# Performance work log

Measured on AMD Instinct MI355X. Metric: run time of the kernel, lower is better.

## Reference

```python
import jax, jax.numpy as jnp
import numpy as np
from jax import lax

W = 65536  # wavelength batch
L = 64     # number of stacked layers
N_IN = 1.0
N_OUT = 1.45
PURITY = 0.87
CD_SCALE = 32980.0  # mdeg conversion, as in source
LN10 = 2.302585092994046


def setup_inputs() -> dict:
    key = jax.random.key(0)
    ks = jax.random.split(key, 9)
    wl = jnp.linspace(0.4, 0.8, W, dtype=jnp.float32)  # microns, matches wl_range*1e-6 usage
    thickP = jax.random.normal(ks[0], (L,), jnp.float32) * 2.0

    def u(k, lo, hi):
        return lo + (hi - lo) * jax.random.uniform(k, (W, L), jnp.float32)

    return {
        "wl": wl,
        "thickP": thickP,
        "mind": jnp.float32(20.0),   # nm
        "maxd": jnp.float32(300.0),  # nm
        "eps_c_re": u(ks[1], 1.8, 4.5),
        "eps_c_im": u(ks[2], 0.0, 0.08),
        "kappa_c_re": u(ks[3], -5e-3, 5e-3),
        "kappa_c_im": u(ks[4], -5e-3, 5e-3),
        "eps_a_re": u(ks[5], 1.8, 4.5),
        "eps_a_im": u(ks[6], 0.0, 0.08),
        "kappa_a_re": u(ks[7], -5e-3, 5e-3),
        "kappa_a_im": u(ks[8], -5e-3, 5e-3),
    }


def _chain(Ms):
    # Ms: [L, W, 2, 2] complex; sequential layer chain-multiply (TMM recursion)
    eye = jnp.broadcast_to(jnp.eye(2, dtype=Ms.dtype), (Ms.shape[1], 2, 2))

    def step(carry, Ml):
        return jnp.einsum('wij,wjk->wik', carry, Ml), None

    Mt, _ = lax.scan(step, eye, Ms)
    return Mt  # [W, 2, 2]


def _absorbance(eps, kappa, sigma, k0, d):
    # Circular eigenmode TMM for Pasteur (isotropic chiral) layers at normal incidence.
    # eps, kappa: [W, L] complex relative quantities; k0: [W]; d: [L] meters.
    n0 = jnp.sqrt(eps)                       # background index, also wave admittance
    n_sig = n0 + sigma * kappa               # circular eigenmode index n +/- kappa
    delta = k0[:, None] * n_sig * d[None, :]  # [W, L] phase thickness
    c = jnp.cos(delta)
    s = jnp.sin(delta)
    Y = n0
    # characteristic matrix per layer: [[cos d, i sin d / Y], [i Y sin d, cos d]]
    M = jnp.stack([jnp.stack([c, 1j * s / Y], axis=-1),
                   jnp.stack([1j * Y * s, c], axis=-1)], axis=-2)  # [W, L, 2, 2]
    Mt = _chain(jnp.transpose(M, (1, 0, 2, 3)))
    m00, m01 = Mt[:, 0, 0], Mt[:, 0, 1]
    m10, m11 = Mt[:, 1, 0], Mt[:, 1, 1]
    denom = N_IN * (m00 + m01 * N_OUT) + (m10 + m11 * N_OUT)
    t = 2.0 * N_IN / denom
    T = (N_OUT / N_IN) * (jnp.abs(t) ** 2)
    return -jnp.log(T + 1e-12) / LN10  # absorbance per handedness


def _stack_cd_abs(eps_re, eps_im, kap_re, kap_im, k0, d):
    eps = (eps_re + 1j * eps_im).astype(jnp.complex64)
    kap = (kap_re + 1j * kap_im).astype(jnp.complex64)
    A_r = _absorbance(eps, kap, +1.0, k0, d)  # RCP
    A_l = _absorbance(eps, kap, -1.0, k0, d)  # LCP
    return A_l - A_r, 0.5 * (A_l + A_r)


def reference(wl, thickP, mind, maxd, eps_c_re, eps_c_im, kappa_c_re, kappa_c_im,
              eps_a_re, eps_a_im, kappa_a_re, kappa_a_im):
    d = (jax.nn.sigmoid(thickP) * (maxd - mind) + mind) * 1e-9  # [L] meters
    k0 = (2.0 * np.float32(3.1415926)) / (wl * 1e-6)             # [W]
    cd_c, abs_c = _stack_cd_abs(eps_c_re, eps_c_im, kappa_c_re, kappa_c_im, k0, d)
    cd_a, abs_a = _stack_cd_abs(eps_a_re, eps_a_im, kappa_a_re, kappa_a_im, k0, d)
    scale = (2.0 * PURITY - 1.0) * CD_SCALE
    return (cd_c * scale, cd_a * scale, abs_c, abs_a)
```

## Files before the change

### kernel.cpp

```cpp
#include <hip/hip_runtime.h>
#include <math.h>

#define LTOT 64
#define GL   8
#define LPL  (LTOT / GL)

#define INV2PI  0.15915494309189535f
#define LOG2E   1.4426950408889634f
#define LOG10_2 0.30102999566398120f

struct cpx { float r, i; };
struct Mat { cpx e00, e01, e10, e11; };

__device__ __forceinline__ cpx cmul(cpx a, cpx b) {
    return { fmaf(a.r, b.r, -a.i * b.i), fmaf(a.r, b.i, a.i * b.r) };
}
__device__ __forceinline__ cpx cmadd(cpx a, cpx b, cpx c) {
    return { fmaf(a.r, b.r, fmaf(-a.i, b.i, c.r)),
             fmaf(a.r, b.i, fmaf( a.i, b.r, c.i)) };
}
__device__ __forceinline__ Mat mmul(const Mat& A, const Mat& B) {
    Mat C;
    C.e00 = cmadd(A.e01, B.e10, cmul(A.e00, B.e00));
    C.e01 = cmadd(A.e01, B.e11, cmul(A.e00, B.e01));
    C.e10 = cmadd(A.e11, B.e10, cmul(A.e10, B.e00));
    C.e11 = cmadd(A.e11, B.e11, cmul(A.e10, B.e01));
    return C;
}
__device__ __forceinline__ void csqrt_inv(cpx z, cpx& n0, float& inv) {
    float m = __builtin_amdgcn_sqrtf(fmaf(z.r, z.r, z.i * z.i));
    float x = 0.5f * (m + z.r);
    float t = __builtin_amdgcn_rsqf(x);
    n0.r = x * t;
    n0.i = 0.5f * z.i * t;
    inv  = __builtin_amdgcn_rcpf(m);
}

__device__ __forceinline__ void accum(Mat& P, bool first, float xrev, float y,
                                      cpx n0, float inv_n0sq) {
    float rf = __builtin_amdgcn_fractf(xrev);
    float s_ = __builtin_amdgcn_sinf(rf);
    float c_ = __builtin_amdgcn_cosf(rf);
    float y2 = y * y;
    float chv = fmaf(y2, fmaf(y2, 0.0416666667f, 0.5f), 1.0f);
    float shv = y * fmaf(y2, fmaf(y2, 0.0083333333f, 0.1666666667f), 1.0f);
    cpx cc = { c_ * chv, -s_ * shv };
    cpx ss = { s_ * chv,  c_ * shv };
    cpx qq = { (ss.r * n0.r + ss.i * n0.i) * inv_n0sq,
               (ss.i * n0.r - ss.r * n0.i) * inv_n0sq };
    cpx m01 = { -qq.i, qq.r };
    cpx p   = cmul(n0, ss);
    cpx m10 = { -p.i, p.r };
    if (first) {
        P.e00 = cc; P.e01 = m01; P.e10 = m10; P.e11 = cc;
    } else {
        Mat C;
        C.e00 = cmadd(P.e01, m10, cmul(P.e00, cc));
        C.e01 = cmadd(P.e01, cc,  cmul(P.e00, m01));
        C.e10 = cmadd(P.e11, m10, cmul(P.e10, cc));
        C.e11 = cmadd(P.e11, cc,  cmul(P.e10, m01));
        P = C;
    }
}

__device__ __forceinline__ Mat shfl_mat(const Mat& M, int mask) {
    Mat R;
    R.e00.r = __shfl_xor(M.e00.r, mask); R.e00.i = __shfl_xor(M.e00.i, mask);
    R.e01.r = __shfl_xor(M.e01.r, mask); R.e01.i = __shfl_xor(M.e01.i, mask);
    R.e10.r = __shfl_xor(M.e10.r, mask); R.e10.i = __shfl_xor(M.e10.i, mask);
    R.e11.r = __shfl_xor(M.e11.r, mask); R.e11.i = __shfl_xor(M.e11.i, mask);
    return R;
}

__global__ __launch_bounds__(256, 4) void chiral_kernel(
    const float* __restrict__ wl,  const float* __restrict__ thickP,
    const float* __restrict__ mindp, const float* __restrict__ maxdp,
    const float* __restrict__ ecr, const float* __restrict__ eci,
    const float* __restrict__ kcr, const float* __restrict__ kci,
    const float* __restrict__ ear, const float* __restrict__ eai,
    const float* __restrict__ kar, const float* __restrict__ kai,
    float* __restrict__ out, int W)
{
    int t = blockIdx.x * blockDim.x + threadIdx.x;
    int w = t >> 3;
    int j = t & 7;
    if (w >= W) return;

    size_t rowbase = (size_t)w * LTOT + (size_t)(LPL * j);

    float4 Ltp[2], Lecr[2], Leci[2], Lkcr[2], Lkci[2], Lear[2], Leai[2], Lkar[2], Lkai[2];
    #pragma unroll
    for (int h = 0; h < 2; h++) {
        size_t b = rowbase + 4 * h;
        Ltp[h]  = *reinterpret_cast<const float4*>(thickP + LPL * j + 4 * h);
        Lecr[h] = *reinterpret_cast<const float4*>(ecr + b);
        Leci[h] = *reinterpret_cast<const float4*>(eci + b);
        Lkcr[h] = *reinterpret_cast<const float4*>(kcr + b);
        Lkci[h] = *reinterpret_cast<const float4*>(kci + b);
        Lear[h] = *reinterpret_cast<const float4*>(ear + b);
        Leai[h] = *reinterpret_cast<const float4*>(eai + b);
        Lkar[h] = *reinterpret_cast<const float4*>(kar + b);
        Lkai[h] = *reinterpret_cast<const float4*>(kai + b);
    }

    float lo = mindp[0], hi = maxdp[0];
    float k0 = 6.2831852e6f * __builtin_amdgcn_rcpf(wl[w]);

    Mat P[4];

    #pragma unroll
    for (int h = 0; h < 2; h++) {
        const float* ptp  = reinterpret_cast<const float*>(&Ltp[h]);
        const float* pecr = reinterpret_cast<const float*>(&Lecr[h]);
        const float* peci = reinterpret_cast<const float*>(&Leci[h]);
        const float* pkcr = reinterpret_cast<const float*>(&Lkcr[h]);
        const float* pkci = reinterpret_cast<const float*>(&Lkci[h]);
        const float* pear = reinterpret_cast<const float*>(&Lear[h]);
        const float* peai = reinterpret_cast<const float*>(&Leai[h]);
        const float* pkar = reinterpret_cast<const float*>(&Lkar[h]);
        const float* pkai = reinterpret_cast<const float*>(&Lkai[h]);

        #pragma unroll
        for (int q = 0; q < 4; q++) {
            bool first = (h == 0 && q == 0);
            float tr = ptp[q];
            float sg = __builtin_amdgcn_rcpf(1.0f + __builtin_amdgcn_exp2f(-tr * LOG2E));
            float d  = fmaf(sg, (hi - lo), lo) * 1e-9f;
            float kd = k0 * d;

            {
                cpx e  = { pecr[q], peci[q] };
                cpx kp = { pkcr[q], pkci[q] };
                cpx n0; float inv;
                csqrt_inv(e, n0, inv);
                float ar = kd * n0.r, ai = kd * n0.i;
                float br = kd * kp.r, bi = kd * kp.i;
                accum(P[0], first, (ar + br) * INV2PI, ai + bi, n0, inv);
                accum(P[1], first, (ar - br) * INV2PI, ai - bi, n0, inv);
            }
            {
                cpx e  = { pear[q], peai[q] };
                cpx kp = { pkar[q], pkai[q] };
                cpx n0; float inv;
                csqrt_inv(e, n0, inv);
                float ar = kd * n0.r, ai = kd * n0.i;
                float br = kd * kp.r, bi = kd * kp.i;
                accum(P[2], first, (ar + br) * INV2PI, ai + bi, n0, inv);
                accum(P[3], first, (ar - br) * INV2PI, ai - bi, n0, inv);
            }
        }
    }

    #pragma unroll
    for (int m = 1; m < GL; m <<= 1) {
        bool up = (j & m) != 0;
        #pragma unroll
        for (int ch = 0; ch < 4; ch++) {
            Mat O = shfl_mat(P[ch], m);
            Mat Lf, Rt;
            Lf.e00 = up ? O.e00 : P[ch].e00; Lf.e01 = up ? O.e01 : P[ch].e01;
            Lf.e10 = up ? O.e10 : P[ch].e10; Lf.e11 = up ? O.e11 : P[ch].e11;
            Rt.e00 = up ? P[ch].e00 : O.e00; Rt.e01 = up ? P[ch].e01 : O.e01;
            Rt.e10 = up ? P[ch].e10 : O.e10; Rt.e11 = up ? P[ch].e11 : O.e11;
            P[ch] = mmul(Lf, Rt);
        }
    }

    if (j == 0) {
        float A[4];
        #pragma unroll
        for (int ch = 0; ch < 4; ch++) {
            float dr = P[ch].e00.r + 1.45f * P[ch].e01.r + P[ch].e10.r + 1.45f * P[ch].e11.r;
            float di = P[ch].e00.i + 1.45f * P[ch].e01.i + P[ch].e10.i + 1.45f * P[ch].e11.i;
            float den = fmaf(dr, dr, di * di);
            float T = 5.8f * __builtin_amdgcn_rcpf(den);
            A[ch] = -__builtin_amdgcn_logf(T + 1e-12f) * LOG10_2;
        }
        const float SC = (2.0f * 0.87f - 1.0f) * 32980.0f;
        out[0 * W + w] = (A[1] - A[0]) * SC;
        out[1 * W + w] = (A[3] - A[2]) * SC;
        out[2 * W + w] = 0.5f * (A[1] + A[0]);
        out[3 * W + w] = 0.5f * (A[3] + A[2]);
    }
}

extern "C" void kernel_launch(void* const* d_in, const int* in_sizes, int n_in,
                              void* d_out, int out_size, void* d_ws, size_t ws_size,
                              hipStream_t stream) {
    const float* wl     = (const float*)d_in[0];
    const float* thickP = (const float*)d_in[1];
    const float* mind   = (const float*)d_in[2];
    const float* maxd   = (const float*)d_in[3];
    const float* ecr    = (const float*)d_in[4];
    const float* eci    = (const float*)d_in[5];
    const float* kcr    = (const float*)d_in[6];
    const float* kci    = (const float*)d_in[7];
    const float* ear    = (const float*)d_in[8];
    const float* eai    = (const float*)d_in[9];
    const float* kar    = (const float*)d_in[10];
    const float* kai    = (const float*)d_in[11];
    float* out = (float*)d_out;

    int W = in_sizes[0];
    int threads = W * GL;
    int block = 256;
    int grid = (threads + block - 1) / block;
    chiral_kernel<<<grid, block, 0, stream>>>(wl, thickP, mind, maxd,
                                              ecr, eci, kcr, kci,
                                              ear, eai, kar, kai, out, W);
}
```

Measured before the change: 180.1 us.

## Pack RCP/LCP handedness into float2 vectors and share trig via angle addition

Processes both circular handedness channels together in packed f32x2 vectors so the compiler can emit packed FP32 ops (v_pk_fma/v_pk_mul on CDNA). The real phase's sin/cos is computed once per layer and the small kappa term is expanded with a short Taylor series, which removes two of the four transcendental sin/cos evaluations. The matrix product uses the symmetric layer structure ([[c, i s/Y],[i Y s, c]]) and stores i-scaled off-diagonals so no separate negation is needed. The risks are extra register pressure from the paired state and a small loss of accuracy from the truncated Taylor series in kappa.

Result: faster. 174.1 us (-3.3%).

```diff
diff --git a/kernel.cpp b/kernel.cpp
--- a/kernel.cpp
+++ b/kernel.cpp
@@ -1,74 +1,103 @@
 #include <hip/hip_runtime.h>
 #include <math.h>
 
+typedef float f32x2 __attribute__((ext_vector_type(2)));
+
 #define LTOT 64
 #define GL   8
-#define LPL  (LTOT / GL)
+#define LPL  8
 
 #define INV2PI  0.15915494309189535f
 #define LOG2E   1.4426950408889634f
 #define LOG10_2 0.30102999566398120f
 
-struct cpx { float r, i; };
-struct Mat { cpx e00, e01, e10, e11; };
-
-__device__ __forceinline__ cpx cmul(cpx a, cpx b) {
-    return { fmaf(a.r, b.r, -a.i * b.i), fmaf(a.r, b.i, a.i * b.r) };
-}
-__device__ __forceinline__ cpx cmadd(cpx a, cpx b, cpx c) {
-    return { fmaf(a.r, b.r, fmaf(-a.i, b.i, c.r)),
-             fmaf(a.r, b.i, fmaf( a.i, b.r, c.i)) };
-}
-__device__ __forceinline__ Mat mmul(const Mat& A, const Mat& B) {
-    Mat C;
-    C.e00 = cmadd(A.e01, B.e10, cmul(A.e00, B.e00));
-    C.e01 = cmadd(A.e01, B.e11, cmul(A.e00, B.e01));
-    C.e10 = cmadd(A.e11, B.e10, cmul(A.e10, B.e00));
-    C.e11 = cmadd(A.e11, B.e11, cmul(A.e10, B.e01));
-    return C;
-}
-__device__ __forceinline__ void csqrt_inv(cpx z, cpx& n0, float& inv) {
-    float m = __builtin_amdgcn_sqrtf(fmaf(z.r, z.r, z.i * z.i));
-    float x = 0.5f * (m + z.r);
-    float t = __builtin_amdgcn_rsqf(x);
-    n0.r = x * t;
-    n0.i = 0.5f * z.i * t;
-    inv  = __builtin_amdgcn_rcpf(m);
-}
-
-__device__ __forceinline__ void accum(Mat& P, bool first, float xrev, float y,
-                                      cpx n0, float inv_n0sq) {
-    float rf = __builtin_amdgcn_fractf(xrev);
-    float s_ = __builtin_amdgcn_sinf(rf);
-    float c_ = __builtin_amdgcn_cosf(rf);
-    float y2 = y * y;
-    float chv = fmaf(y2, fmaf(y2, 0.0416666667f, 0.5f), 1.0f);
-    float shv = y * fmaf(y2, fmaf(y2, 0.0083333333f, 0.1666666667f), 1.0f);
-    cpx cc = { c_ * chv, -s_ * shv };
-    cpx ss = { s_ * chv,  c_ * shv };
-    cpx qq = { (ss.r * n0.r + ss.i * n0.i) * inv_n0sq,
-               (ss.i * n0.r - ss.r * n0.i) * inv_n0sq };
-    cpx m01 = { -qq.i, qq.r };
-    cpx p   = cmul(n0, ss);
-    cpx m10 = { -p.i, p.r };
+struct C2 { f32x2 r, i; };
+struct M2 { C2 A, B, C, D; };
+
+__device__ __forceinline__ f32x2 shx(f32x2 v, int m) {
+    f32x2 r;
+    r.x = __shfl_xor(v.x, m);
+    r.y = __shfl_xor(v.y, m);
+    return r;
+}
+
+__device__ __forceinline__ void layer_stack(M2& M, bool first, float kd,
+                                            float er, float ei, float kr, float ki) {
+    float mm  = __builtin_amdgcn_sqrtf(fmaf(er, er, ei * ei));
+    float x   = 0.5f * (mm + er);
+    float rx  = __builtin_amdgcn_rsqf(x);
+    float n0r = x * rx;
+    float n0i = 0.5f * ei * rx;
+    float inv = __builtin_amdgcn_rcpf(mm);
+
+    float ar = kd * n0r, ai = kd * n0i;
+    float br = kd * kr,  bi = kd * ki;
+
+    float rf = __builtin_amdgcn_fractf(ar * INV2PI);
+    float sa = __builtin_amdgcn_sinf(rf);
+    float ca = __builtin_amdgcn_cosf(rf);
+    float b2 = br * br;
+    float sb = br * fmaf(b2, -0.16666667f, 1.0f);
+    float cb = fmaf(b2, -0.5f, 1.0f);
+    float u = sa * cb, v = ca * sb, wq = ca * cb, zq = sa * sb;
+
+    f32x2 S, Cx, Y;
+    S.x = u + v;   S.y = u - v;
+    Cx.x = wq - zq; Cx.y = wq + zq;
+    Y.x = ai + bi; Y.y = ai - bi;
+
+    f32x2 y2 = Y * Y;
+    f32x2 ch = (y2 * 0.041666667f + 0.5f) * y2 + 1.0f;
+    f32x2 sh = Y * ((y2 * 0.0083333333f + 0.16666667f) * y2 + 1.0f);
+
+    f32x2 c_r = Cx * ch;
+    f32x2 c_i = -(S * sh);
+    f32x2 s_r = S * ch;
+    f32x2 s_i = Cx * sh;
+
+    f32x2 q_r = (s_r * n0r + s_i * n0i) * inv;
+    f32x2 q_i = (s_i * n0r - s_r * n0i) * inv;
+    f32x2 p_r = s_r * n0r - s_i * n0i;
+    f32x2 p_i = s_i * n0r + s_r * n0i;
+
     if (first) {
-        P.e00 = cc; P.e01 = m01; P.e10 = m10; P.e11 = cc;
+        M.A.r = c_r; M.A.i = c_i;
+        M.B.r = q_r; M.B.i = q_i;
+        M.C.r = p_r; M.C.i = p_i;
+        M.D.r = c_r; M.D.i = c_i;
     } else {
-        Mat C;
-        C.e00 = cmadd(P.e01, m10, cmul(P.e00, cc));
-        C.e01 = cmadd(P.e01, cc,  cmul(P.e00, m01));
-        C.e10 = cmadd(P.e11, m10, cmul(P.e10, cc));
-        C.e11 = cmadd(P.e11, cc,  cmul(P.e10, m01));
-        P = C;
-    }
-}
-
-__device__ __forceinline__ Mat shfl_mat(const Mat& M, int mask) {
-    Mat R;
-    R.e00.r = __shfl_xor(M.e00.r, mask); R.e00.i = __shfl_xor(M.e00.i, mask);
-    R.e01.r = __shfl_xor(M.e01.r, mask); R.e01.i = __shfl_xor(M.e01.i, mask);
-    R.e10.r = __shfl_xor(M.e10.r, mask); R.e10.i = __shfl_xor(M.e10.i, mask);
-    R.e11.r = __shfl_xor(M.e11.r, mask); R.e11.i = __shfl_xor(M.e11.i, mask);
+        f32x2 nAr = M.A.r*c_r - M.A.i*c_i - M.B.r*p_r + M.B.i*p_i;
+        f32x2 nAi = M.A.r*c_i + M.A.i*c_r - M.B.r*p_i - M.B.i*p_r;
+        f32x2 nBr = M.A.r*q_r - M.A.i*q_i + M.B.r*c_r - M.B.i*c_i;
+        f32x2 nBi = M.A.r*q_i + M.A.i*q_r + M.B.r*c_i + M.B.i*c_r;
+        f32x2 nCr = M.C.r*c_r - M.C.i*c_i + M.D.r*p_r - M.D.i*p_i;
+        f32x2 nCi = M.C.r*c_i + M.C.i*c_r + M.D.r*p_i + M.D.i*p_r;
+        f32x2 nDr = M.D.r*c_r - M.D.i*c_i - M.C.r*q_r + M.C.i*q_i;
+        f32x2 nDi = M.D.r*c_i + M.D.i*c_r - M.C.r*q_i - M.C.i*q_r;
+        M.A.r = nAr; M.A.i = nAi; M.B.r = nBr; M.B.i = nBi;
+        M.C.r = nCr; M.C.i = nCi; M.D.r = nDr; M.D.i = nDi;
+    }
+}
+
+__device__ __forceinline__ void combine(M2& L, const M2& R) {
+    f32x2 nAr = L.A.r*R.A.r - L.A.i*R.A.i - L.B.r*R.C.r + L.B.i*R.C.i;
+    f32x2 nAi = L.A.r*R.A.i + L.A.i*R.A.r - L.B.r*R.C.i - L.B.i*R.C.r;
+    f32x2 nBr = L.A.r*R.B.r - L.A.i*R.B.i + L.B.r*R.D.r - L.B.i*R.D.i;
+    f32x2 nBi = L.A.r*R.B.i + L.A.i*R.B.r + L.B.r*R.D.i + L.B.i*R.D.r;
+    f32x2 nCr = L.C.r*R.A.r - L.C.i*R.A.i + L.D.r*R.C.r - L.D.i*R.C.i;
+    f32x2 nCi = L.C.r*R.A.i + L.C.i*R.A.r + L.D.r*R.C.i + L.D.i*R.C.r;
+    f32x2 nDr = L.D.r*R.D.r - L.D.i*R.D.i - L.C.r*R.B.r + L.C.i*R.B.i;
+    f32x2 nDi = L.D.r*R.D.i + L.D.i*R.D.r - L.C.r*R.B.i - L.C.i*R.B.r;
+    L.A.r = nAr; L.A.i = nAi; L.B.r = nBr; L.B.i = nBi;
+    L.C.r = nCr; L.C.i = nCi; L.D.r = nDr; L.D.i = nDi;
+}
+
+__device__ __forceinline__ M2 shfl_m2(const M2& M, int m) {
+    M2 R;
+    R.A.r = shx(M.A.r, m); R.A.i = shx(M.A.i, m);
+    R.B.r = shx(M.B.r, m); R.B.i = shx(M.B.i, m);
+    R.C.r = shx(M.C.r, m); R.C.i = shx(M.C.i, m);
+    R.D.r = shx(M.D.r, m); R.D.i = shx(M.D.i, m);
     return R;
 }
 
@@ -106,7 +135,7 @@
     float lo = mindp[0], hi = maxdp[0];
     float k0 = 6.2831852e6f * __builtin_amdgcn_rcpf(wl[w]);
 
-    Mat P[4];
+    M2 Mc, Ma;
 
     #pragma unroll
     for (int h = 0; h < 2; h++) {
@@ -128,59 +157,37 @@
             float d  = fmaf(sg, (hi - lo), lo) * 1e-9f;
             float kd = k0 * d;
 
-            {
-                cpx e  = { pecr[q], peci[q] };
-                cpx kp = { pkcr[q], pkci[q] };
-                cpx n0; float inv;
-                csqrt_inv(e, n0, inv);
-                float ar = kd * n0.r, ai = kd * n0.i;
-                float br = kd * kp.r, bi = kd * kp.i;
-                accum(P[0], first, (ar + br) * INV2PI, ai + bi, n0, inv);
-                accum(P[1], first, (ar - br) * INV2PI, ai - bi, n0, inv);
-            }
-            {
-                cpx e  = { pear[q], peai[q] };
-                cpx kp = { pkar[q], pkai[q] };
-                cpx n0; float inv;
-                csqrt_inv(e, n0, inv);
-                float ar = kd * n0.r, ai = kd * n0.i;
-                float br = kd * kp.r, bi = kd * kp.i;
-                accum(P[2], first, (ar + br) * INV2PI, ai + bi, n0, inv);
-                accum(P[3], first, (ar - br) * INV2PI, ai - bi, n0, inv);
-            }
+            layer_stack(Mc, first, kd, pecr[q], peci[q], pkcr[q], pkci[q]);
+            layer_stack(Ma, first, kd, pear[q], peai[q], pkar[q], pkai[q]);
         }
     }
 
     #pragma unroll
     for (int m = 1; m < GL; m <<= 1) {
-        bool up = (j & m) != 0;
-        #pragma unroll
-        for (int ch = 0; ch < 4; ch++) {
-            Mat O = shfl_mat(P[ch], m);
-            Mat Lf, Rt;
-            Lf.e00 = up ? O.e00 : P[ch].e00; Lf.e01 = up ? O.e01 : P[ch].e01;
-            Lf.e10 = up ? O.e10 : P[ch].e10; Lf.e11 = up ? O.e11 : P[ch].e11;
-            Rt.e00 = up ? P[ch].e00 : O.e00; Rt.e01 = up ? P[ch].e01 : O.e01;
-            Rt.e10 = up ? P[ch].e10 : O.e10; Rt.e11 = up ? P[ch].e11 : O.e11;
-            P[ch] = mmul(Lf, Rt);
-        }
+        M2 Oc = shfl_m2(Mc, m);
+        M2 Oa = shfl_m2(Ma, m);
+        combine(Mc, Oc);
+        combine(Ma, Oa);
     }
 
     if (j == 0) {
-        float A[4];
-        #pragma unroll
-        for (int ch = 0; ch < 4; ch++) {
-            float dr = P[ch].e00.r + 1.45f * P[ch].e01.r + P[ch].e10.r + 1.45f * P[ch].e11.r;
-            float di = P[ch].e00.i + 1.45f * P[ch].e01.i + P[ch].e10.i + 1.45f * P[ch].e11.i;
-            float den = fmaf(dr, dr, di * di);
-            float T = 5.8f * __builtin_amdgcn_rcpf(den);
-            A[ch] = -__builtin_amdgcn_logf(T + 1e-12f) * LOG10_2;
-        }
+        const float NOUT = 1.45f;
+        f32x2 drc = Mc.A.r + NOUT * Mc.D.r - NOUT * Mc.B.i - Mc.C.i;
+        f32x2 dic = Mc.A.i + NOUT * Mc.D.i + NOUT * Mc.B.r + Mc.C.r;
+        f32x2 dra = Ma.A.r + NOUT * Ma.D.r - NOUT * Ma.B.i - Ma.C.i;
+        f32x2 dia = Ma.A.i + NOUT * Ma.D.i + NOUT * Ma.B.r + Ma.C.r;
+        f32x2 denc = drc * drc + dic * dic;
+        f32x2 dena = dra * dra + dia * dia;
+        float Arc = -LOG10_2 * __builtin_amdgcn_logf(5.8f * __builtin_amdgcn_rcpf(denc.x) + 1e-12f);
+        float Alc = -LOG10_2 * __builtin_amdgcn_logf(5.8f * __builtin_amdgcn_rcpf(denc.y) + 1e-12f);
+        float Ara = -LOG10_2 * __builtin_amdgcn_logf(5.8f * __builtin_amdgcn_rcpf(dena.x) + 1e-12f);
+        float Ala = -LOG10_2 * __builtin_amdgcn_logf(5.8f * __builtin_amdgcn_rcpf(dena.y) + 1e-12f);
+
         const float SC = (2.0f * 0.87f - 1.0f) * 32980.0f;
-        out[0 * W + w] = (A[1] - A[0]) * SC;
-        out[1 * W + w] = (A[3] - A[2]) * SC;
-        out[2 * W + w] = 0.5f * (A[1] + A[0]);
-        out[3 * W + w] = 0.5f * (A[3] + A[2]);
+        out[0 * W + w] = (Alc - Arc) * SC;
+        out[1 * W + w] = (Ala - Ara) * SC;
+        out[2 * W + w] = 0.5f * (Alc + Arc);
+        out[3 * W + w] = 0.5f * (Ala + Ara);
     }
 }
 
```
